# Kernel optimization log

Measured on AMD Instinct MI355X. Metric: run time of the kernel, lower is better.

The kernel has to match this reference:

```python
import jax, jax.numpy as jnp
import numpy as np

EPS = 1e-8

def rms_norm(x, scale):
    # norm(2,-1)/sqrt(d); x / (rms + eps) * scale
    d = x.shape[-1]
    norm = jnp.sqrt(jnp.sum(x * x, axis=-1, keepdims=True))
    rms = norm / jnp.sqrt(jnp.asarray(d, x.dtype))
    return scale * (x / (rms + EPS))

def setup_inputs() -> dict:
    key = jax.random.key(0)
    B, N, C, FF = 2, 2048, 1024, 4096
    ks = jax.random.split(key, 12)
    s = 0.02
    return {
        "x":  jax.random.normal(ks[0], (B, N, C), jnp.float32),
        "wq": jax.random.normal(ks[1], (C, C), jnp.float32) * s,
        "bq": jnp.zeros((C,), jnp.float32),
        "wk": jax.random.normal(ks[2], (C, C), jnp.float32) * s,
        "bk": jnp.zeros((C,), jnp.float32),
        "wv": jax.random.normal(ks[3], (C, C), jnp.float32) * s,
        "bv": jnp.zeros((C,), jnp.float32),
        "wo": jax.random.normal(ks[4], (C, C), jnp.float32) * s,
        "bo": jnp.zeros((C,), jnp.float32),
        "scale1": jnp.ones((C,), jnp.float32),
        "scale2": jnp.ones((C,), jnp.float32),
        "w1": jax.random.normal(ks[5], (C, FF), jnp.float32) * s,
        "b1": jnp.zeros((FF,), jnp.float32),
        "w2": jax.random.normal(ks[6], (FF, C), jnp.float32) * s,
        "b2": jnp.zeros((C,), jnp.float32),
    }

def reference(x, wq, bq, wk, bk, wv, bv, wo, bo, scale1, scale2, w1, b1, w2, b2):
    B, N, C = x.shape
    H = 16
    D = C // H

    residual = x
    xn = rms_norm(x, scale1)

    def heads(y):  # [B,N,C] -> [B,H,N,D]
        return y.reshape(B, N, H, D).transpose(0, 2, 1, 3)

    q = heads(xn @ wq + bq)
    k = heads(xn @ wk + bk)
    v = heads(xn @ wv + bv)

    # apply_rotary_pos_emb with cos=sin=1: q' = q - roll(q,1,-1), same for k
    q = q - jnp.roll(q, 1, axis=-1)
    k = k - jnp.roll(k, 1, axis=-1)

    # explicit attention (no causal mask in original)
    scores = jnp.einsum('bhnd,bhmd->bhnm', q, k) / jnp.sqrt(jnp.asarray(D, x.dtype))
    probs = jax.nn.softmax(scores, axis=-1)
    attn = jnp.einsum('bhnm,bhmd->bhnd', probs, v)
    attn = attn.transpose(0, 2, 1, 3).reshape(B, N, C)
    attn = attn @ wo + bo

    x = residual + attn
    residual = x
    xn = rms_norm(x, scale2)
    h = jax.nn.gelu(xn @ w1 + b1, approximate=False)  # torch GELU default = exact
    ffn_out = h @ w2 + b2
    return residual + ffn_out
```

## Files before the change

### kernel.cpp

```cpp
#include <hip/hip_runtime.h>
#include <hip/hip_bf16.h>
#include <math.h>

typedef unsigned short u16;
typedef short s16x8 __attribute__((ext_vector_type(8)));
typedef __bf16 bf16x8v __attribute__((ext_vector_type(8)));
typedef float f32x4 __attribute__((ext_vector_type(4)));
typedef unsigned short u16x4 __attribute__((ext_vector_type(4)));

struct Ptr4 { float* p[4]; };
struct TW4 { const float* w[4]; u16* o[4]; };

__device__ __forceinline__ u16 f2b(float f) {
    __hip_bfloat16 h = __float2bfloat16(f);
    return __builtin_bit_cast(u16, h);
}

__device__ __forceinline__ f32x4 mfma16(s16x8 a, s16x8 b, f32x4 c) {
    return __builtin_amdgcn_mfma_f32_16x16x32_bf16(
        __builtin_bit_cast(bf16x8v, a), __builtin_bit_cast(bf16x8v, b), c, 0, 0, 0);
}

__device__ __forceinline__ void gl_lds16(const void* g, void* l) {
    typedef const unsigned int __attribute__((address_space(1))) * gp_t;
    typedef unsigned int __attribute__((address_space(3))) * lp_t;
    __builtin_amdgcn_global_load_lds((gp_t)(unsigned long long)g,
                                     (lp_t)(unsigned int)(unsigned long long)l,
                                     16, 0, 0);
}

__device__ __forceinline__ float gelu_fast(float v) {
    float u = 1.5957691216f * (v + 0.044715f * v * v * v);
    return v / (1.f + __expf(-u));
}

__global__ __launch_bounds__(256) void transpose_w(const float* __restrict__ W,
                                                   u16* __restrict__ Wt,
                                                   int K, int N) {
    __shared__ u16 tile[32][33];
    const int tx = threadIdx.x & 31, ty = threadIdx.x >> 5;
    const int n0 = blockIdx.x * 32, k0 = blockIdx.y * 32;
#pragma unroll
    for (int i = 0; i < 32; i += 8)
        tile[ty + i][tx] = f2b(W[(size_t)(k0 + ty + i) * N + n0 + tx]);
    __syncthreads();
#pragma unroll
    for (int i = 0; i < 32; i += 8)
        Wt[(size_t)(n0 + ty + i) * K + k0 + tx] = tile[tx][ty + i];
}

__global__ __launch_bounds__(256) void transpose_w4(TW4 io) {
    __shared__ u16 tile[32][33];
    const int z = blockIdx.z;
    const float* W = io.w[z];
    u16* Wt = io.o[z];
    const int tx = threadIdx.x & 31, ty = threadIdx.x >> 5;
    const int n0 = blockIdx.x * 32, k0 = blockIdx.y * 32;
#pragma unroll
    for (int i = 0; i < 32; i += 8)
        tile[ty + i][tx] = f2b(W[(size_t)(k0 + ty + i) * 1024 + n0 + tx]);
    __syncthreads();
#pragma unroll
    for (int i = 0; i < 32; i += 8)
        Wt[(size_t)(n0 + ty + i) * 1024 + k0 + tx] = tile[tx][ty + i];
}

__global__ __launch_bounds__(256) void transpose_v(const u16* __restrict__ qkv,
                                                   u16* __restrict__ vT) {
    __shared__ u16 tile[32][33];
    const int tx = threadIdx.x & 31, ty = threadIdx.x >> 5;
    const int n0 = blockIdx.x * 32, d0 = blockIdx.y * 32, bh = blockIdx.z;
    const int b = bh >> 4, h = bh & 15;
#pragma unroll
    for (int i = 0; i < 32; i += 8)
        tile[ty + i][tx] =
            qkv[(size_t)(b * 2048 + n0 + ty + i) * 3072 + 2048 + h * 64 + d0 + tx];
    __syncthreads();
#pragma unroll
    for (int i = 0; i < 32; i += 8)
        vT[((size_t)bh * 64 + d0 + ty + i) * 2048 + n0 + tx] = tile[tx][ty + i];
}

__global__ __launch_bounds__(256) void rmsnorm_kernel(const float* __restrict__ x,
                                                      const float* __restrict__ scale,
                                                      u16* __restrict__ out) {
    __shared__ float red[4];
    const int t = threadIdx.x, row = blockIdx.x;
    const float4* xr = (const float4*)(x + (size_t)row * 1024);
    float4 v = xr[t];
    float ss = v.x * v.x + v.y * v.y + v.z * v.z + v.w * v.w;
#pragma unroll
    for (int off = 1; off < 64; off <<= 1) ss += __shfl_xor(ss, off);
    if ((t & 63) == 0) red[t >> 6] = ss;
    __syncthreads();
    float tot = red[0] + red[1] + red[2] + red[3];
    float inv = 1.f / (sqrtf(tot * (1.f / 1024.f)) + 1e-8f);
    const float4* sr = (const float4*)scale;
    float4 s = sr[t];
    u16x4 o;
    o[0] = f2b(v.x * inv * s.x);
    o[1] = f2b(v.y * inv * s.y);
    o[2] = f2b(v.z * inv * s.z);
    o[3] = f2b(v.w * inv * s.w);
    ((u16x4*)(out + (size_t)row * 1024))[t] = o;
}

template <int EPI>
__global__ __launch_bounds__(256) void gemm_kernel(const u16* __restrict__ A,
                                                   const u16* __restrict__ Bt,
                                                   const float* __restrict__ bias,
                                                   const float* __restrict__ bias2,
                                                   const float* __restrict__ bias3,
                                                   const float* __restrict__ resid,
                                                   void* __restrict__ outp,
                                                   int M, int N, int K) {
    __shared__ __align__(16) u16 As[128 * 32];
    __shared__ __align__(16) u16 Bs[128 * 32];
    const int t = threadIdx.x, lane = t & 63;
    const int w = t >> 6, wm = (w >> 1) * 64, wn = (w & 1) * 64;
    const int c = lane & 15, qd = lane >> 4;
    const int n0 = blockIdx.x * 128, m0 = blockIdx.y * 128;

    const int sch = ((t & 3) ^ ((t >> 3) & 3)) * 8;
    const u16* Ag = A + (size_t)(m0 + (t >> 2)) * K + sch;
    const u16* Bg = Bt + (size_t)(n0 + (t >> 2)) * K + sch;
    const size_t half = (size_t)64 * K;
    const int fsw = ((c >> 1) & 3);

    f32x4 acc[4][4] = {};
    for (int kt = 0; kt < K; kt += 32) {
        __syncthreads();
        gl_lds16(Ag, &As[t * 8]);
        gl_lds16(Ag + half, &As[2048 + t * 8]);
        gl_lds16(Bg, &Bs[t * 8]);
        gl_lds16(Bg + half, &Bs[2048 + t * 8]);
        Ag += 32;
        Bg += 32;
        __syncthreads();
        s16x8 a[4], b[4];
#pragma unroll
        for (int im = 0; im < 4; im++)
            a[im] = *(const s16x8*)&As[(wm + im * 16 + c) * 32 + ((qd ^ fsw) * 8)];
#pragma unroll
        for (int jn = 0; jn < 4; jn++)
            b[jn] = *(const s16x8*)&Bs[(wn + jn * 16 + c) * 32 + ((qd ^ fsw) * 8)];
#pragma unroll
        for (int im = 0; im < 4; im++)
#pragma unroll
            for (int jn = 0; jn < 4; jn++)
                acc[im][jn] = mfma16(a[im], b[jn], acc[im][jn]);
    }

    if (EPI == 3) {
        const int colbase = n0 + wn;
        const bool isq = colbase < 1024, isv = colbase >= 2048;
        const float* bp = isq ? bias : (isv ? bias3 : bias2);
        const int cb = colbase & 1023;
#pragma unroll
        for (int im = 0; im < 4; im++)
#pragma unroll
            for (int r = 0; r < 4; r++) {
                float v[4], sh[4], b15[4];
#pragma unroll
                for (int jn = 0; jn < 4; jn++)
                    v[jn] = acc[im][jn][r] + bp[cb + jn * 16 + c];
#pragma unroll
                for (int jn = 0; jn < 4; jn++) {
                    sh[jn] = __shfl(v[jn], qd * 16 + ((c + 15) & 15));
                    b15[jn] = __shfl(v[jn], qd * 16 + 15);
                }
                const int rowg = m0 + wm + im * 16 + qd * 4 + r;
#pragma unroll
                for (int jn = 0; jn < 4; jn++) {
                    float prev = (c == 0) ? b15[(jn + 3) & 3] : sh[jn];
                    float ov = isv ? v[jn] : (v[jn] - prev);
                    if (isq) ov *= 0.125f;
                    ((u16*)outp)[(size_t)rowg * N + colbase + jn * 16 + c] = f2b(ov);
                }
            }
        return;
    }

#pragma unroll
    for (int im = 0; im < 4; im++) {
#pragma unroll
        for (int jn = 0; jn < 4; jn++) {
            const int colg = n0 + wn + jn * 16 + c;
            const float bv = bias[colg];
#pragma unroll
            for (int r = 0; r < 4; r++) {
                const int rowg = m0 + wm + im * 16 + qd * 4 + r;
                const size_t off = (size_t)rowg * N + colg;
                float v = acc[im][jn][r] + bv;
                if (EPI == 0) {
                    ((u16*)outp)[off] = f2b(v);
                } else if (EPI == 1) {
                    ((float*)outp)[off] = v + resid[off];
                } else {
                    ((u16*)outp)[off] = f2b(gelu_fast(v));
                }
            }
        }
    }
}

__global__ __launch_bounds__(256) void gemm_splitk(const u16* __restrict__ A,
                                                   const u16* __restrict__ Bt,
                                                   Ptr4 parts,
                                                   int N, int Ktot, int Kc) {
    __shared__ __align__(16) u16 As[128 * 32];
    __shared__ __align__(16) u16 Bs[128 * 32];
    const int t = threadIdx.x, lane = t & 63;
    const int w = t >> 6, wm = (w >> 1) * 64, wn = (w & 1) * 64;
    const int c = lane & 15, qd = lane >> 4;
    const int n0 = blockIdx.x * 128, m0 = blockIdx.y * 128;
    const int z = blockIdx.z;
    float* out = parts.p[z];

    const int sch = ((t & 3) ^ ((t >> 3) & 3)) * 8;
    const u16* Ag = A + (size_t)(m0 + (t >> 2)) * Ktot + z * Kc + sch;
    const u16* Bg = Bt + (size_t)(n0 + (t >> 2)) * Ktot + z * Kc + sch;
    const size_t half = (size_t)64 * Ktot;
    const int fsw = ((c >> 1) & 3);

    f32x4 acc[4][4] = {};
    for (int kt = 0; kt < Kc; kt += 32) {
        __syncthreads();
        gl_lds16(Ag, &As[t * 8]);
        gl_lds16(Ag + half, &As[2048 + t * 8]);
        gl_lds16(Bg, &Bs[t * 8]);
        gl_lds16(Bg + half, &Bs[2048 + t * 8]);
        Ag += 32;
        Bg += 32;
        __syncthreads();
        s16x8 a[4], b[4];
#pragma unroll
        for (int im = 0; im < 4; im++)
            a[im] = *(const s16x8*)&As[(wm + im * 16 + c) * 32 + ((qd ^ fsw) * 8)];
#pragma unroll
        for (int jn = 0; jn < 4; jn++)
            b[jn] = *(const s16x8*)&Bs[(wn + jn * 16 + c) * 32 + ((qd ^ fsw) * 8)];
#pragma unroll
        for (int im = 0; im < 4; im++)
#pragma unroll
            for (int jn = 0; jn < 4; jn++)
                acc[im][jn] = mfma16(a[im], b[jn], acc[im][jn]);
    }

#pragma unroll
    for (int im = 0; im < 4; im++)
#pragma unroll
        for (int jn = 0; jn < 4; jn++) {
            const int colg = n0 + wn + jn * 16 + c;
#pragma unroll
            for (int r = 0; r < 4; r++) {
                const int rowg = m0 + wm + im * 16 + qd * 4 + r;
                out[(size_t)rowg * N + colg] = acc[im][jn][r];
            }
        }
}

template <int S, bool NORM>
__global__ __launch_bounds__(256) void reduce_kernel(Ptr4 parts,
                                                     const float* __restrict__ bias,
                                                     const float* __restrict__ resid,
                                                     const float* __restrict__ scale,
                                                     float* __restrict__ yout,
                                                     u16* __restrict__ xnout) {
    __shared__ float red[4];
    const int t = threadIdx.x, row = blockIdx.x;
    const size_t base = (size_t)row * 1024;
    float4 v = ((const float4*)(resid + base))[t];
    float4 bv = ((const float4*)bias)[t];
    v.x += bv.x; v.y += bv.y; v.z += bv.z; v.w += bv.w;
#pragma unroll
    for (int s = 0; s < S; s++) {
        float4 pv = ((const float4*)(parts.p[s] + base))[t];
        v.x += pv.x; v.y += pv.y; v.z += pv.z; v.w += pv.w;
    }
    ((float4*)(yout + base))[t] = v;
    if (NORM) {
        float ss = v.x * v.x + v.y * v.y + v.z * v.z + v.w * v.w;
#pragma unroll
        for (int off = 1; off < 64; off <<= 1) ss += __shfl_xor(ss, off);
        if ((t & 63) == 0) red[t >> 6] = ss;
        __syncthreads();
        float tot = red[0] + red[1] + red[2] + red[3];
        float inv = 1.f / (sqrtf(tot * (1.f / 1024.f)) + 1e-8f);
        float4 s = ((const float4*)scale)[t];
        u16x4 o;
        o[0] = f2b(v.x * inv * s.x);
        o[1] = f2b(v.y * inv * s.y);
        o[2] = f2b(v.z * inv * s.z);
        o[3] = f2b(v.w * inv * s.w);
        ((u16x4*)(xnout + base))[t] = o;
    }
}

__global__ __launch_bounds__(256) void attn_kernel(const u16* __restrict__ qkv,
                                                   const u16* __restrict__ vT,
                                                   u16* __restrict__ attn) {
    __shared__ __align__(16) u16 Qs[128 * 64];
    __shared__ __align__(16) u16 Ks[2][64 * 64];
    __shared__ __align__(16) u16 Vs[2][64 * 64];
    __shared__ __align__(16) u16 Ps[4 * 32 * 64];

    const int t = threadIdx.x, lane = t & 63, w = t >> 6;
    const int c = lane & 15, qd = lane >> 4;
    const int bh = blockIdx.y, b = bh >> 4, h = bh & 15;
    const int q0 = blockIdx.x * 128;
    const size_t rowbase = (size_t)b * 2048;

    const u16* qg = qkv + (rowbase + q0) * 3072 + h * 64;
    const u16* kg = qkv + rowbase * 3072 + 1024 + h * 64;
    const u16* vg = vT + (size_t)bh * 64 * 2048;

    const int srow = t >> 3;
    const int sch = (t & 7) ^ (srow & 7);

    const u16* kptr = kg + (size_t)srow * 3072 + sch * 8;
    const u16* vptr = vg + (size_t)srow * 2048 + sch * 8;

#pragma unroll
    for (int i = 0; i < 4; i++)
        gl_lds16(qg + (size_t)(srow + i * 32) * 3072 + sch * 8, &Qs[t * 8 + i * 2048]);
    gl_lds16(kptr, &Ks[0][t * 8]);
    gl_lds16(kptr + (size_t)32 * 3072, &Ks[0][2048 + t * 8]);
    gl_lds16(vptr, &Vs[0][t * 8]);
    gl_lds16(vptr + (size_t)32 * 2048, &Vs[0][2048 + t * 8]);
    __syncthreads();

    s16x8 qf[2][2];
#pragma unroll
    for (int im = 0; im < 2; im++)
#pragma unroll
        for (int ks = 0; ks < 2; ks++)
            qf[im][ks] = *(const s16x8*)&Qs[(w * 32 + im * 16 + c) * 64 +
                                            (((ks * 4 + qd) ^ (c & 7)) * 8)];

    float lsum[2][4] = {};
    f32x4 o[2][4] = {};
    u16* Pw = &Ps[w * 32 * 64];

    for (int it = 0; it < 32; it++) {
        const int buf = it & 1;
        const u16* Kb = Ks[buf];
        const u16* Vb = Vs[buf];

        if (it + 1 < 32) {
            u16* Kn = Ks[buf ^ 1];
            u16* Vn = Vs[buf ^ 1];
            const size_t ko = (size_t)(it + 1) * 64 * 3072;
            const size_t vo = (size_t)(it + 1) * 64;
            gl_lds16(kptr + ko, &Kn[t * 8]);
            gl_lds16(kptr + ko + (size_t)32 * 3072, &Kn[2048 + t * 8]);
            gl_lds16(vptr + vo, &Vn[t * 8]);
            gl_lds16(vptr + vo + (size_t)32 * 2048, &Vn[2048 + t * 8]);
        }

        s16x8 kf[2][4], vf[2][4];
#pragma unroll
        for (int ks = 0; ks < 2; ks++)
#pragma unroll
            for (int j = 0; j < 4; j++) {
                const int rrow = j * 16 + c;
                const int sw = ((ks * 4 + qd) ^ (rrow & 7)) * 8;
                kf[ks][j] = *(const s16x8*)&Kb[rrow * 64 + sw];
                vf[ks][j] = *(const s16x8*)&Vb[rrow * 64 + sw];
            }

#pragma unroll
        for (int im = 0; im < 2; im++) {
            f32x4 sc[4] = {};
#pragma unroll
            for (int ks = 0; ks < 2; ks++)
#pragma unroll
                for (int jn = 0; jn < 4; jn++)
                    sc[jn] = mfma16(qf[im][ks], kf[ks][jn], sc[jn]);
#pragma unroll
            for (int r = 0; r < 4; r++) {
                const int prow = im * 16 + qd * 4 + r;
                float s = 0.f;
#pragma unroll
                for (int jn = 0; jn < 4; jn++) {
                    float p = __expf(sc[jn][r]);
                    s += p;
                    Pw[prow * 64 + (((jn * 2 + (c >> 3)) ^ (prow & 7)) * 8) + (c & 7)] =
                        f2b(p);
                }
                lsum[im][r] += s;
            }
        }

#pragma unroll
        for (int im = 0; im < 2; im++)
#pragma unroll
            for (int ks = 0; ks < 2; ks++) {
                s16x8 pf = *(const s16x8*)&Pw[(im * 16 + c) * 64 +
                                              (((ks * 4 + qd) ^ (c & 7)) * 8)];
#pragma unroll
                for (int jd = 0; jd < 4; jd++)
                    o[im][jd] = mfma16(pf, vf[ks][jd], o[im][jd]);
            }
        __syncthreads();
    }

#pragma unroll
    for (int im = 0; im < 2; im++)
#pragma unroll
        for (int r = 0; r < 4; r++)
#pragma unroll
            for (int off2 = 1; off2 < 16; off2 <<= 1)
                lsum[im][r] += __shfl_xor(lsum[im][r], off2);

    const int orow_base = b * 2048 + q0 + w * 32;
#pragma unroll
    for (int im = 0; im < 2; im++)
#pragma unroll
        for (int r = 0; r < 4; r++) {
            const float inv = 1.f / lsum[im][r];
            const int grow = orow_base + im * 16 + qd * 4 + r;
#pragma unroll
            for (int jd = 0; jd < 4; jd++)
                attn[(size_t)grow * 1024 + h * 64 + jd * 16 + c] =
                    f2b(o[im][jd][r] * inv);
        }
}

extern "C" void kernel_launch(void* const* d_in, const int* in_sizes, int n_in,
                              void* d_out, int out_size, void* d_ws, size_t ws_size,
                              hipStream_t stream) {
    const float* x = (const float*)d_in[0];
    const float* wq = (const float*)d_in[1];
    const float* bq = (const float*)d_in[2];
    const float* wk = (const float*)d_in[3];
    const float* bk = (const float*)d_in[4];
    const float* wv = (const float*)d_in[5];
    const float* bv = (const float*)d_in[6];
    const float* wo = (const float*)d_in[7];
    const float* bo = (const float*)d_in[8];
    const float* scale1 = (const float*)d_in[9];
    const float* scale2 = (const float*)d_in[10];
    const float* w1 = (const float*)d_in[11];
    const float* b1 = (const float*)d_in[12];
    const float* w2 = (const float*)d_in[13];
    const float* b2 = (const float*)d_in[14];
    float* out = (float*)d_out;

    char* ws = (char*)d_ws;
    size_t off = 0;
    auto alloc = [&](size_t bytes) -> char* {
        char* p = ws + off;
        off += (bytes + 255) & ~(size_t)255;
        return p;
    };
    u16* wqkvT = (u16*)alloc((size_t)3072 * 1024 * 2);
    u16* woT   = (u16*)alloc((size_t)1024 * 1024 * 2);
    u16* w1T   = (u16*)alloc((size_t)4096 * 1024 * 2);
    u16* w2T   = (u16*)alloc((size_t)1024 * 4096 * 2);
    u16* xn    = (u16*)alloc((size_t)4096 * 1024 * 2);
    u16* qkv   = (u16*)alloc((size_t)4096 * 3072 * 2);
    u16* vT    = (u16*)alloc((size_t)32 * 64 * 2048 * 2);
    u16* attnb = (u16*)alloc((size_t)4096 * 1024 * 2);
    float* y1  = (float*)alloc((size_t)4096 * 1024 * 4);
    u16* hbuf  = (u16*)alloc((size_t)4096 * 4096 * 2);

    const size_t SPLIT = (size_t)4096 * 1024;
    Ptr4 po; po.p[0] = (float*)qkv; po.p[1] = (float*)qkv + SPLIT;
    po.p[2] = nullptr; po.p[3] = nullptr;
    Ptr4 pf; pf.p[0] = (float*)xn; pf.p[1] = (float*)xn + SPLIT;
    pf.p[2] = (float*)xn + 2 * SPLIT; pf.p[3] = (float*)wqkvT;

    dim3 blk(256);

    TW4 tw;
    tw.w[0] = wq; tw.o[0] = wqkvT;
    tw.w[1] = wk; tw.o[1] = wqkvT + (size_t)1024 * 1024;
    tw.w[2] = wv; tw.o[2] = wqkvT + (size_t)2048 * 1024;
    tw.w[3] = wo; tw.o[3] = woT;
    transpose_w4<<<dim3(32, 32, 4), blk, 0, stream>>>(tw);
    transpose_w<<<dim3(128, 32), blk, 0, stream>>>(w1, w1T, 1024, 4096);
    transpose_w<<<dim3(32, 128), blk, 0, stream>>>(w2, w2T, 4096, 1024);

    rmsnorm_kernel<<<4096, blk, 0, stream>>>(x, scale1, xn);
    gemm_kernel<3><<<dim3(24, 32), blk, 0, stream>>>(xn, wqkvT, bq, bk, bv, nullptr, qkv, 4096, 3072, 1024);
    transpose_v<<<dim3(64, 2, 32), blk, 0, stream>>>(qkv, vT);
    attn_kernel<<<dim3(16, 32), blk, 0, stream>>>(qkv, vT, attnb);
    gemm_splitk<<<dim3(8, 32, 2), blk, 0, stream>>>(attnb, woT, po, 1024, 1024, 512);
    reduce_kernel<2, true><<<4096, blk, 0, stream>>>(po, bo, x, scale2, y1, xn);
    gemm_kernel<2><<<dim3(32, 32), blk, 0, stream>>>(xn, w1T, b1, nullptr, nullptr, nullptr, hbuf, 4096, 4096, 1024);
    gemm_splitk<<<dim3(8, 32, 4), blk, 0, stream>>>(hbuf, w2T, pf, 1024, 4096, 1024);
    reduce_kernel<4, false><<<4096, blk, 0, stream>>>(pf, b2, y1, nullptr, out, nullptr);
}
```

Baseline: 405.4 us.

## Fold rotary shift and q scaling into weights; load Q directly to registers

The rotary difference (q - roll(q)) and the 1/sqrt(D) scale are linear, so they are folded into the transposed Wq/Wk weights and a precomputed bias. This lets the QKV GEMM use the plain bias epilogue instead of the shuffle-based one. The attention kernel also drops the Q shared-memory tile, loads Q fragments straight from global memory into registers, and sets a 3-blocks-per-CU occupancy hint. The cost is slightly more weight-prep work per call, and bf16 rounding now happens on the folded weights rather than after the subtraction.

```diff
diff --git a/kernel.cpp b/kernel.cpp
--- a/kernel.cpp
+++ b/kernel.cpp
@@ -9,7 +9,7 @@
 typedef unsigned short u16x4 __attribute__((ext_vector_type(4)));
 
 struct Ptr4 { float* p[4]; };
-struct TW4 { const float* w[4]; u16* o[4]; };
+struct TW4 { const float* w[4]; u16* o[4]; int mode[4]; };
 
 __device__ __forceinline__ u16 f2b(float f) {
     __hip_bfloat16 h = __float2bfloat16(f);
@@ -54,15 +54,37 @@
     const int z = blockIdx.z;
     const float* W = io.w[z];
     u16* Wt = io.o[z];
+    const int mode = io.mode[z];
     const int tx = threadIdx.x & 31, ty = threadIdx.x >> 5;
     const int n0 = blockIdx.x * 32, k0 = blockIdx.y * 32;
-#pragma unroll
-    for (int i = 0; i < 32; i += 8)
-        tile[ty + i][tx] = f2b(W[(size_t)(k0 + ty + i) * 1024 + n0 + tx]);
+    const int n = n0 + tx;
+    const int np = (n & ~63) | ((n + 63) & 63);
+    const float s = (mode == 1) ? 0.125f : 1.f;
+#pragma unroll
+    for (int i = 0; i < 32; i += 8) {
+        const size_t r = (size_t)(k0 + ty + i) * 1024;
+        float v = W[r + n];
+        if (mode) v = (v - W[r + np]) * s;
+        tile[ty + i][tx] = f2b(v);
+    }
     __syncthreads();
 #pragma unroll
     for (int i = 0; i < 32; i += 8)
         Wt[(size_t)(n0 + ty + i) * 1024 + k0 + tx] = tile[tx][ty + i];
+}
+
+__global__ __launch_bounds__(256) void prep_bias(const float* __restrict__ bq,
+                                                 const float* __restrict__ bk,
+                                                 const float* __restrict__ bv,
+                                                 float* __restrict__ bqkv) {
+    const int i = blockIdx.x * 256 + threadIdx.x;
+    const int d = i & 1023;
+    const int dp = (d & ~63) | ((d + 63) & 63);
+    float v;
+    if (i < 1024) v = 0.125f * (bq[d] - bq[dp]);
+    else if (i < 2048) v = bk[d] - bk[dp];
+    else v = bv[d];
+    bqkv[i] = v;
 }
 
 __global__ __launch_bounds__(256) void transpose_v(const u16* __restrict__ qkv,
@@ -109,8 +131,6 @@
 __global__ __launch_bounds__(256) void gemm_kernel(const u16* __restrict__ A,
                                                    const u16* __restrict__ Bt,
                                                    const float* __restrict__ bias,
-                                                   const float* __restrict__ bias2,
-                                                   const float* __restrict__ bias3,
                                                    const float* __restrict__ resid,
                                                    void* __restrict__ outp,
                                                    int M, int N, int K) {
@@ -149,36 +169,6 @@
 #pragma unroll
             for (int jn = 0; jn < 4; jn++)
                 acc[im][jn] = mfma16(a[im], b[jn], acc[im][jn]);
-    }
-
-    if (EPI == 3) {
-        const int colbase = n0 + wn;
-        const bool isq = colbase < 1024, isv = colbase >= 2048;
-        const float* bp = isq ? bias : (isv ? bias3 : bias2);
-        const int cb = colbase & 1023;
-#pragma unroll
-        for (int im = 0; im < 4; im++)
-#pragma unroll
-            for (int r = 0; r < 4; r++) {
-                float v[4], sh[4], b15[4];
-#pragma unroll
-                for (int jn = 0; jn < 4; jn++)
-                    v[jn] = acc[im][jn][r] + bp[cb + jn * 16 + c];
-#pragma unroll
-                for (int jn = 0; jn < 4; jn++) {
-                    sh[jn] = __shfl(v[jn], qd * 16 + ((c + 15) & 15));
-                    b15[jn] = __shfl(v[jn], qd * 16 + 15);
-                }
-                const int rowg = m0 + wm + im * 16 + qd * 4 + r;
-#pragma unroll
-                for (int jn = 0; jn < 4; jn++) {
-                    float prev = (c == 0) ? b15[(jn + 3) & 3] : sh[jn];
-                    float ov = isv ? v[jn] : (v[jn] - prev);
-                    if (isq) ov *= 0.125f;
-                    ((u16*)outp)[(size_t)rowg * N + colbase + jn * 16 + c] = f2b(ov);
-                }
-            }
-        return;
     }
 
 #pragma unroll
@@ -297,10 +287,9 @@
     }
 }
 
-__global__ __launch_bounds__(256) void attn_kernel(const u16* __restrict__ qkv,
-                                                   const u16* __restrict__ vT,
-                                                   u16* __restrict__ attn) {
-    __shared__ __align__(16) u16 Qs[128 * 64];
+__global__ __launch_bounds__(256, 3) void attn_kernel(const u16* __restrict__ qkv,
+                                                      const u16* __restrict__ vT,
+                                                      u16* __restrict__ attn) {
     __shared__ __align__(16) u16 Ks[2][64 * 64];
     __shared__ __align__(16) u16 Vs[2][64 * 64];
     __shared__ __align__(16) u16 Ps[4 * 32 * 64];
@@ -311,7 +300,6 @@
     const int q0 = blockIdx.x * 128;
     const size_t rowbase = (size_t)b * 2048;
 
-    const u16* qg = qkv + (rowbase + q0) * 3072 + h * 64;
     const u16* kg = qkv + rowbase * 3072 + 1024 + h * 64;
     const u16* vg = vT + (size_t)bh * 64 * 2048;
 
@@ -321,22 +309,22 @@
     const u16* kptr = kg + (size_t)srow * 3072 + sch * 8;
     const u16* vptr = vg + (size_t)srow * 2048 + sch * 8;
 
-#pragma unroll
-    for (int i = 0; i < 4; i++)
-        gl_lds16(qg + (size_t)(srow + i * 32) * 3072 + sch * 8, &Qs[t * 8 + i * 2048]);
     gl_lds16(kptr, &Ks[0][t * 8]);
     gl_lds16(kptr + (size_t)32 * 3072, &Ks[0][2048 + t * 8]);
     gl_lds16(vptr, &Vs[0][t * 8]);
     gl_lds16(vptr + (size_t)32 * 2048, &Vs[0][2048 + t * 8]);
+
+    s16x8 qf[2][2];
+    {
+        const u16* qg = qkv + (rowbase + q0 + w * 32) * 3072 + h * 64;
+#pragma unroll
+        for (int im = 0; im < 2; im++)
+#pragma unroll
+            for (int ks = 0; ks < 2; ks++)
+                qf[im][ks] = *(const s16x8*)&qg[(size_t)(im * 16 + c) * 3072 +
+                                                ks * 32 + qd * 8];
+    }
     __syncthreads();
-
-    s16x8 qf[2][2];
-#pragma unroll
-    for (int im = 0; im < 2; im++)
-#pragma unroll
-        for (int ks = 0; ks < 2; ks++)
-            qf[im][ks] = *(const s16x8*)&Qs[(w * 32 + im * 16 + c) * 64 +
-                                            (((ks * 4 + qd) ^ (c & 7)) * 8)];
 
     float lsum[2][4] = {};
     f32x4 o[2][4] = {};
@@ -458,6 +446,7 @@
     u16* woT   = (u16*)alloc((size_t)1024 * 1024 * 2);
     u16* w1T   = (u16*)alloc((size_t)4096 * 1024 * 2);
     u16* w2T   = (u16*)alloc((size_t)1024 * 4096 * 2);
+    float* bqkv = (float*)alloc(3072 * 4);
     u16* xn    = (u16*)alloc((size_t)4096 * 1024 * 2);
     u16* qkv   = (u16*)alloc((size_t)4096 * 3072 * 2);
     u16* vT    = (u16*)alloc((size_t)32 * 64 * 2048 * 2);
@@ -474,21 +463,22 @@
     dim3 blk(256);
 
     TW4 tw;
-    tw.w[0] = wq; tw.o[0] = wqkvT;
-    tw.w[1] = wk; tw.o[1] = wqkvT + (size_t)1024 * 1024;
-    tw.w[2] = wv; tw.o[2] = wqkvT + (size_t)2048 * 1024;
-    tw.w[3] = wo; tw.o[3] = woT;
+    tw.w[0] = wq; tw.o[0] = wqkvT;                          tw.mode[0] = 1;
+    tw.w[1] = wk; tw.o[1] = wqkvT + (size_t)1024 * 1024;    tw.mode[1] = 2;
+    tw.w[2] = wv; tw.o[2] = wqkvT + (size_t)2048 * 1024;    tw.mode[2] = 0;
+    tw.w[3] = wo; tw.o[3] = woT;                            tw.mode[3] = 0;
     transpose_w4<<<dim3(32, 32, 4), blk, 0, stream>>>(tw);
     transpose_w<<<dim3(128, 32), blk, 0, stream>>>(w1, w1T, 1024, 4096);
     transpose_w<<<dim3(32, 128), blk, 0, stream>>>(w2, w2T, 4096, 1024);
+    prep_bias<<<12, blk, 0, stream>>>(bq, bk, bv, bqkv);
 
     rmsnorm_kernel<<<4096, blk, 0, stream>>>(x, scale1, xn);
-    gemm_kernel<3><<<dim3(24, 32), blk, 0, stream>>>(xn, wqkvT, bq, bk, bv, nullptr, qkv, 4096, 3072, 1024);
+    gemm_kernel<0><<<dim3(24, 32), blk, 0, stream>>>(xn, wqkvT, bqkv, nullptr, qkv, 4096, 3072, 1024);
     transpose_v<<<dim3(64, 2, 32), blk, 0, stream>>>(qkv, vT);
     attn_kernel<<<dim3(16, 32), blk, 0, stream>>>(qkv, vT, attnb);
     gemm_splitk<<<dim3(8, 32, 2), blk, 0, stream>>>(attnb, woT, po, 1024, 1024, 512);
     reduce_kernel<2, true><<<4096, blk, 0, stream>>>(po, bo, x, scale2, y1, xn);
-    gemm_kernel<2><<<dim3(32, 32), blk, 0, stream>>>(xn, w1T, b1, nullptr, nullptr, nullptr, hbuf, 4096, 4096, 1024);
+    gemm_kernel<2><<<dim3(32, 32), blk, 0, stream>>>(xn, w1T, b1, nullptr, hbuf, 4096, 4096, 1024);
     gemm_splitk<<<dim3(8, 32, 4), blk, 0, stream>>>(hbuf, w2T, pf, 1024, 4096, 1024);
     reduce_kernel<4, false><<<4096, blk, 0, stream>>>(pf, b2, y1, nullptr, out, nullptr);
 }
```

After: 403.5 us. No clear change (-0.5%).
